# Kernel tuning notes

Hardware: AMD Instinct MI355X
Metric: run time of the kernel (lower is better)

## Reference

```python
import jax, jax.numpy as jnp
import numpy as np

N = 50000
E = 600000
D_IN = 128
D_HID = 128
D_OUT = 40
BN_EPS = 1e-5


def setup_inputs() -> dict:
    key = jax.random.key(0)
    ks = jax.random.split(key, 16)
    g = lambda k, *s: (jax.random.normal(k, s, jnp.float32) * 0.05)
    return {
        "x": jax.random.normal(ks[0], (N, D_IN), jnp.float32),
        "edge_index": jax.random.randint(ks[1], (2, E), 0, N, dtype=jnp.int64),
        "W0": g(ks[2], D_IN, D_HID), "b0": jnp.zeros((D_HID,), jnp.float32),
        "W1": g(ks[3], D_HID, D_HID), "b1": jnp.zeros((D_HID,), jnp.float32),
        "W2": g(ks[4], D_HID, D_OUT), "b2": jnp.zeros((D_OUT,), jnp.float32),
        "g0": 1.0 + g(ks[5], D_HID), "be0": g(ks[6], D_HID),
        "m0": g(ks[7], D_HID), "v0": 0.5 + jax.random.uniform(ks[8], (D_HID,), jnp.float32),
        "g1": 1.0 + g(ks[9], D_HID), "be1": g(ks[10], D_HID),
        "m1": g(ks[11], D_HID), "v1": 0.5 + jax.random.uniform(ks[12], (D_HID,), jnp.float32),
    }


def reference(x, edge_index, W0, b0, W1, b1, W2, b2,
              g0, be0, m0, v0, g1, be1, m1, v1):
    n = x.shape[0]
    loop = jnp.arange(n, dtype=edge_index.dtype)
    # GCN with self-loops: A_hat = A + I, symmetric normalization
    src = jnp.concatenate([edge_index[0], loop])
    dst = jnp.concatenate([edge_index[1], loop])
    deg = jax.ops.segment_sum(jnp.ones_like(dst, jnp.float32), dst, num_segments=n)
    dinv = jax.lax.rsqrt(jnp.maximum(deg, 1.0))
    norm = dinv[src] * dinv[dst]  # [E+N]

    def conv(h, W, b):
        h = h @ W + b                                   # [N, d_out]
        msg = norm[:, None] * h[src]                    # gather + scale
        return jax.ops.segment_sum(msg, dst, num_segments=n)

    def bn_relu(h, g, be, m, v):
        return jax.nn.relu((h - m) * (g * jax.lax.rsqrt(v + BN_EPS)) + be)

    h = bn_relu(conv(x, W0, b0), g0, be0, m0, v0)
    h = bn_relu(conv(h, W1, b1), g1, be1, m1, v1)
    h = conv(h, W2, b2)
    return jax.nn.log_softmax(h, axis=-1)
```

## Files before the change

kernel.cpp:

```cpp
#include <hip/hip_runtime.h>
#include <math.h>

#define BN_EPS 1e-5f
#define CAP 96

typedef unsigned short ushort_t;
typedef __attribute__((ext_vector_type(8))) short short8;
typedef __attribute__((ext_vector_type(4))) float floatx4;

__device__ inline ushort_t f2b(float f) {
    unsigned u = __float_as_uint(f);
    unsigned r = u + 0x7FFFu + ((u >> 16) & 1u);
    return (ushort_t)(r >> 16);
}
__device__ inline float b2f(ushort_t b) { return __uint_as_float(((unsigned)b) << 16); }
__device__ inline float2 u2f2(unsigned u) {
    return make_float2(b2f((ushort_t)(u & 0xffffu)), b2f((ushort_t)(u >> 16)));
}


__global__ void fill_ell(const int* __restrict__ ei, int* __restrict__ cnt,
                         int* __restrict__ ell, int E) {
    int e = blockIdx.x * blockDim.x + threadIdx.x;
    if (e >= E) return;
    int s = ei[e];
    int d = ei[E + e];
    int p = atomicAdd(&cnt[d], 1);
    if (p < CAP) ell[(size_t)d * CAP + p] = s;
}

__global__ void make_dinv(const int* __restrict__ cnt, float* __restrict__ dinv, int n) {
    int i = blockIdx.x * blockDim.x + threadIdx.x;
    if (i < n) dinv[i] = rsqrtf((float)(cnt[i] + 1));
}

__global__ __launch_bounds__(256) void cast_wt_all(const float* __restrict__ W0,
                                                   const float* __restrict__ W1,
                                                   const float* __restrict__ W2,
                                                   ushort_t* __restrict__ Wt0,
                                                   ushort_t* __restrict__ Wt1,
                                                   ushort_t* __restrict__ Wt2) {
    int i = blockIdx.x * 256 + threadIdx.x;
    if (i < 16384) {
        int n = i >> 7, k = i & 127;
        Wt0[i] = f2b(W0[k * 128 + n]);
    } else if (i < 32768) {
        int j = i - 16384;
        int n = j >> 7, k = j & 127;
        Wt1[j] = f2b(W1[k * 128 + n]);
    } else if (i < 40960) {
        int j = i - 32768;
        int n = j >> 7, k = j & 127;
        Wt2[j] = (n < 40) ? f2b(W2[k * 40 + n]) : (ushort_t)0;
    }
}

template<int NT, bool AF32>
__global__ __launch_bounds__(256) void gemm_mfma(const void* __restrict__ Av,
                                                 const ushort_t* __restrict__ Wt,
                                                 const float* __restrict__ bias,
                                                 const float* __restrict__ dinv,
                                                 ushort_t* __restrict__ C,
                                                 int M, int ncols) {
    __shared__ ushort_t As[128 * 128];
    __shared__ ushort_t Ws[NT * 128];
    const int tid = threadIdx.x;
    const int rbase = blockIdx.x * 128;

#pragma unroll
    for (int p = 0; p < 8; ++p) {
        int cid = p * 256 + tid;
        int gr = rbase + (cid >> 4);
        if (AF32) {
            const float* A32 = (const float*)Av;
            float4 f0 = make_float4(0.f, 0.f, 0.f, 0.f), f1 = f0;
            if (gr < M) {
                f0 = *(const float4*)(A32 + (size_t)rbase * 128 + (size_t)cid * 8);
                f1 = *(const float4*)(A32 + (size_t)rbase * 128 + (size_t)cid * 8 + 4);
            }
            union { ushort_t u[8]; uint4 w; } o;
            o.u[0] = f2b(f0.x); o.u[1] = f2b(f0.y); o.u[2] = f2b(f0.z); o.u[3] = f2b(f0.w);
            o.u[4] = f2b(f1.x); o.u[5] = f2b(f1.y); o.u[6] = f2b(f1.z); o.u[7] = f2b(f1.w);
            *(uint4*)(As + cid * 8) = o.w;
        } else {
            const ushort_t* A16 = (const ushort_t*)Av;
            uint4 val = make_uint4(0, 0, 0, 0);
            if (gr < M) val = *(const uint4*)(A16 + (size_t)rbase * 128 + (size_t)cid * 8);
            *(uint4*)(As + cid * 8) = val;
        }
    }
#pragma unroll
    for (int p = 0; p < NT / 16; ++p) {
        int cid = p * 256 + tid;
        *(uint4*)(Ws + cid * 8) = *(const uint4*)(Wt + (size_t)cid * 8);
    }
    __syncthreads();

    const int wave = tid >> 6, lane = tid & 63;
    const int m = lane & 15, quad = lane >> 4;
    constexpr int CT = NT / 16;
    floatx4 acc[2][CT];
#pragma unroll
    for (int rt = 0; rt < 2; ++rt)
#pragma unroll
        for (int ct = 0; ct < CT; ++ct) acc[rt][ct] = (floatx4){0.f, 0.f, 0.f, 0.f};

    const int r0 = wave * 32;
#pragma unroll
    for (int ks = 0; ks < 4; ++ks) {
        short8 a0 = *(const short8*)(As + (r0 + m) * 128 + ks * 32 + quad * 8);
        short8 a1 = *(const short8*)(As + (r0 + 16 + m) * 128 + ks * 32 + quad * 8);
#pragma unroll
        for (int ct = 0; ct < CT; ++ct) {
            short8 b = *(const short8*)(Ws + (ct * 16 + m) * 128 + ks * 32 + quad * 8);
            acc[0][ct] = __builtin_amdgcn_mfma_f32_16x16x32_bf16(a0, b, acc[0][ct], 0, 0, 0);
            acc[1][ct] = __builtin_amdgcn_mfma_f32_16x16x32_bf16(a1, b, acc[1][ct], 0, 0, 0);
        }
    }

    float dsc[2][4];
#pragma unroll
    for (int rt = 0; rt < 2; ++rt)
#pragma unroll
        for (int r = 0; r < 4; ++r) {
            int gr = rbase + r0 + rt * 16 + quad * 4 + r;
            dsc[rt][r] = (gr < M) ? dinv[gr] : 0.f;
        }

    __syncthreads();
#pragma unroll
    for (int rt = 0; rt < 2; ++rt) {
#pragma unroll
        for (int ct = 0; ct < CT; ++ct) {
            int col = ct * 16 + m;
            float bv = (col < ncols) ? bias[col] : 0.f;
#pragma unroll
            for (int r = 0; r < 4; ++r) {
                int row = r0 + rt * 16 + quad * 4 + r;
                As[row * NT + col] = f2b((acc[rt][ct][r] + bv) * dsc[rt][r]);
            }
        }
    }
    __syncthreads();
    constexpr int CPT = 128 * NT / 8 / 256;
#pragma unroll
    for (int p = 0; p < CPT; ++p) {
        int cid = p * 256 + tid;
        int row = cid / (NT / 8);
        int gr = rbase + row;
        if (gr < M)
            *(uint4*)(C + (size_t)gr * NT + (cid % (NT / 8)) * 8) = *(const uint4*)(As + cid * 8);
    }
}

__global__ __launch_bounds__(256) void agg128_bn(const ushort_t* __restrict__ h,
                                                 const int* __restrict__ cnt,
                                                 const int* __restrict__ ell,
                                                 const float* __restrict__ dinv,
                                                 const float* __restrict__ g,
                                                 const float* __restrict__ be,
                                                 const float* __restrict__ m,
                                                 const float* __restrict__ v,
                                                 ushort_t* __restrict__ out, int n) {
    int wv = __builtin_amdgcn_readfirstlane((blockIdx.x * 256 + threadIdx.x) >> 6);
    int lane = threadIdx.x & 63;
    if (wv >= n) return;
    const unsigned* h2 = (const unsigned*)h;
    float dv = dinv[wv];
    float2 hv = u2f2(h2[(size_t)wv * 64 + lane]);
    float ax = hv.x, ay = hv.y;
    int c = min(cnt[wv], CAP);
    const int* row = ell + (size_t)wv * CAP;
    int k = 0;
    for (; k + 8 <= c; k += 8) {
        int s[8];
#pragma unroll
        for (int j = 0; j < 8; ++j) s[j] = row[k + j];
#pragma unroll
        for (int j = 0; j < 8; ++j) {
            float2 t = u2f2(h2[(size_t)s[j] * 64 + lane]);
            ax += t.x;
            ay += t.y;
        }
    }
    if (k < c) {
        int rem = c - k;
        int s[8];
#pragma unroll
        for (int j = 0; j < 8; ++j) {
            int sr = row[k + j];
            s[j] = (j < rem) ? sr : 0;
        }
#pragma unroll
        for (int j = 0; j < 8; ++j) {
            float2 t = u2f2(h2[(size_t)s[j] * 64 + lane]);
            ax += (j < rem) ? t.x : 0.f;
            ay += (j < rem) ? t.y : 0.f;
        }
    }
    ax *= dv;
    ay *= dv;
    int c0 = lane * 2;
    float s0f = g[c0] * rsqrtf(v[c0] + BN_EPS);
    float s1f = g[c0 + 1] * rsqrtf(v[c0 + 1] + BN_EPS);
    float o0 = fmaxf(fmaf(ax - m[c0], s0f, be[c0]), 0.f);
    float o1 = fmaxf(fmaf(ay - m[c0 + 1], s1f, be[c0 + 1]), 0.f);
    unsigned ov = (unsigned)f2b(o0) | ((unsigned)f2b(o1) << 16);
    ((unsigned*)out)[(size_t)wv * 64 + lane] = ov;
}

__global__ __launch_bounds__(256) void agg40_lsm(const ushort_t* __restrict__ h,
                                                 const int* __restrict__ cnt,
                                                 const int* __restrict__ ell,
                                                 const float* __restrict__ dinv,
                                                 float* __restrict__ out, int n) {
    int wv = __builtin_amdgcn_readfirstlane((blockIdx.x * 256 + threadIdx.x) >> 6);
    int lane = threadIdx.x & 63;
    if (wv >= n) return;
    float dv = dinv[wv];
    float acc = b2f(h[(size_t)wv * 64 + lane]);
    int c = min(cnt[wv], CAP);
    const int* row = ell + (size_t)wv * CAP;
    int k = 0;
    for (; k + 8 <= c; k += 8) {
        int s[8];
#pragma unroll
        for (int j = 0; j < 8; ++j) s[j] = row[k + j];
#pragma unroll
        for (int j = 0; j < 8; ++j) acc += b2f(h[(size_t)s[j] * 64 + lane]);
    }
    if (k < c) {
        int rem = c - k;
        int s[8];
#pragma unroll
        for (int j = 0; j < 8; ++j) {
            int sr = row[k + j];
            s[j] = (j < rem) ? sr : 0;
        }
#pragma unroll
        for (int j = 0; j < 8; ++j) {
            float t = b2f(h[(size_t)s[j] * 64 + lane]);
            acc += (j < rem) ? t : 0.f;
        }
    }
    acc *= dv;
    bool act = lane < 40;
    float x = act ? acc : -INFINITY;
    float mx = x;
#pragma unroll
    for (int off = 32; off > 0; off >>= 1) mx = fmaxf(mx, __shfl_xor(mx, off, 64));
    float ex = act ? expf(acc - mx) : 0.f;
    float se = ex;
#pragma unroll
    for (int off = 32; off > 0; off >>= 1) se += __shfl_xor(se, off, 64);
    float r = acc - mx - logf(se);
    if (act) out[(size_t)wv * 40 + lane] = r;
}


extern "C" void kernel_launch(void* const* d_in, const int* in_sizes, int n_in,
                              void* d_out, int out_size, void* d_ws, size_t ws_size,
                              hipStream_t stream) {
    const float* x = (const float*)d_in[0];
    const int* ei = (const int*)d_in[1];
    const float* W0 = (const float*)d_in[2];
    const float* b0 = (const float*)d_in[3];
    const float* W1 = (const float*)d_in[4];
    const float* b1 = (const float*)d_in[5];
    const float* W2 = (const float*)d_in[6];
    const float* b2 = (const float*)d_in[7];
    const float* g0 = (const float*)d_in[8];
    const float* be0 = (const float*)d_in[9];
    const float* m0 = (const float*)d_in[10];
    const float* v0 = (const float*)d_in[11];
    const float* g1 = (const float*)d_in[12];
    const float* be1 = (const float*)d_in[13];
    const float* m1 = (const float*)d_in[14];
    const float* v1 = (const float*)d_in[15];
    float* out = (float*)d_out;

    const int N = in_sizes[0] / 128;
    const int E = in_sizes[1] / 2;

    char* wp = (char*)d_ws;
    auto alloc = [&](size_t bytes) -> char* {
        char* p = wp;
        wp += (bytes + 255) & ~(size_t)255;
        return p;
    };
    int* cnt = (int*)alloc((size_t)N * 4);
    float* dinv = (float*)alloc((size_t)N * 4);
    int* ell = (int*)alloc(((size_t)N * CAP + 8) * 4);
    ushort_t* hA = (ushort_t*)alloc((size_t)N * 128 * 2);
    ushort_t* hB = (ushort_t*)alloc((size_t)N * 128 * 2);
    ushort_t* hA2 = (ushort_t*)alloc((size_t)N * 128 * 2);
    ushort_t* hB2 = (ushort_t*)alloc((size_t)N * 128 * 2);
    ushort_t* hL = (ushort_t*)alloc((size_t)N * 64 * 2);
    ushort_t* Wt0 = (ushort_t*)alloc(128 * 128 * 2);
    ushort_t* Wt1 = (ushort_t*)alloc(128 * 128 * 2);
    ushort_t* Wt2 = (ushort_t*)alloc(64 * 128 * 2);

    hipMemsetAsync(cnt, 0, (size_t)N * 4, stream);
    fill_ell<<<(E + 255) / 256, 256, 0, stream>>>(ei, cnt, ell, E);
    make_dinv<<<(N + 255) / 256, 256, 0, stream>>>(cnt, dinv, N);
    cast_wt_all<<<160, 256, 0, stream>>>(W0, W1, W2, Wt0, Wt1, Wt2);

    int gblocks = (N + 127) / 128;
    gemm_mfma<128, true><<<gblocks, 256, 0, stream>>>(x, Wt0, b0, dinv, hA, N, 128);
    agg128_bn<<<(N + 3) / 4, 256, 0, stream>>>(hA, cnt, ell, dinv, g0, be0, m0, v0, hB, N);
    gemm_mfma<128, false><<<gblocks, 256, 0, stream>>>(hB, Wt1, b1, dinv, hA2, N, 128);
    agg128_bn<<<(N + 3) / 4, 256, 0, stream>>>(hA2, cnt, ell, dinv, g1, be1, m1, v1, hB2, N);
    gemm_mfma<64, false><<<gblocks, 256, 0, stream>>>(hB2, Wt2, b2, dinv, hL, N, 40);
    agg40_lsm<<<(N + 3) / 4, 256, 0, stream>>>(hL, cnt, ell, dinv, out, N);
}
```

Baseline: 241.5 us.

## Fuse ELL build, first GEMM and weight casts into one launch; fold dinv into aggregation

Result: slower. 288.2 us (+19.3%).

```diff
diff --git a/kernel.cpp b/kernel.cpp
--- a/kernel.cpp
+++ b/kernel.cpp
@@ -18,81 +18,31 @@
     return make_float2(b2f((ushort_t)(u & 0xffffu)), b2f((ushort_t)(u >> 16)));
 }
 
-
-__global__ void fill_ell(const int* __restrict__ ei, int* __restrict__ cnt,
-                         int* __restrict__ ell, int E) {
-    int e = blockIdx.x * blockDim.x + threadIdx.x;
-    if (e >= E) return;
-    int s = ei[e];
-    int d = ei[E + e];
-    int p = atomicAdd(&cnt[d], 1);
-    if (p < CAP) ell[(size_t)d * CAP + p] = s;
-}
-
-__global__ void make_dinv(const int* __restrict__ cnt, float* __restrict__ dinv, int n) {
-    int i = blockIdx.x * blockDim.x + threadIdx.x;
-    if (i < n) dinv[i] = rsqrtf((float)(cnt[i] + 1));
-}
-
-__global__ __launch_bounds__(256) void cast_wt_all(const float* __restrict__ W0,
-                                                   const float* __restrict__ W1,
-                                                   const float* __restrict__ W2,
-                                                   ushort_t* __restrict__ Wt0,
-                                                   ushort_t* __restrict__ Wt1,
-                                                   ushort_t* __restrict__ Wt2) {
-    int i = blockIdx.x * 256 + threadIdx.x;
-    if (i < 16384) {
-        int n = i >> 7, k = i & 127;
-        Wt0[i] = f2b(W0[k * 128 + n]);
-    } else if (i < 32768) {
-        int j = i - 16384;
-        int n = j >> 7, k = j & 127;
-        Wt1[j] = f2b(W1[k * 128 + n]);
-    } else if (i < 40960) {
-        int j = i - 32768;
-        int n = j >> 7, k = j & 127;
-        Wt2[j] = (n < 40) ? f2b(W2[k * 40 + n]) : (ushort_t)0;
-    }
-}
-
-template<int NT, bool AF32>
-__global__ __launch_bounds__(256) void gemm_mfma(const void* __restrict__ Av,
-                                                 const ushort_t* __restrict__ Wt,
-                                                 const float* __restrict__ bias,
-                                                 const float* __restrict__ dinv,
-                                                 ushort_t* __restrict__ C,
-                                                 int M, int ncols) {
-    __shared__ ushort_t As[128 * 128];
-    __shared__ ushort_t Ws[NT * 128];
-    const int tid = threadIdx.x;
-    const int rbase = blockIdx.x * 128;
-
-#pragma unroll
-    for (int p = 0; p < 8; ++p) {
-        int cid = p * 256 + tid;
-        int gr = rbase + (cid >> 4);
-        if (AF32) {
-            const float* A32 = (const float*)Av;
-            float4 f0 = make_float4(0.f, 0.f, 0.f, 0.f), f1 = f0;
-            if (gr < M) {
-                f0 = *(const float4*)(A32 + (size_t)rbase * 128 + (size_t)cid * 8);
-                f1 = *(const float4*)(A32 + (size_t)rbase * 128 + (size_t)cid * 8 + 4);
-            }
-            union { ushort_t u[8]; uint4 w; } o;
-            o.u[0] = f2b(f0.x); o.u[1] = f2b(f0.y); o.u[2] = f2b(f0.z); o.u[3] = f2b(f0.w);
-            o.u[4] = f2b(f1.x); o.u[5] = f2b(f1.y); o.u[6] = f2b(f1.z); o.u[7] = f2b(f1.w);
-            *(uint4*)(As + cid * 8) = o.w;
-        } else {
-            const ushort_t* A16 = (const ushort_t*)Av;
-            uint4 val = make_uint4(0, 0, 0, 0);
-            if (gr < M) val = *(const uint4*)(A16 + (size_t)rbase * 128 + (size_t)cid * 8);
-            *(uint4*)(As + cid * 8) = val;
-        }
-    }
+template<int NT, bool AF32, bool SELFW>
+__device__ __forceinline__ void gemm_body(
+    ushort_t* __restrict__ Ws,
+    const void* __restrict__ Av,
+    const void* __restrict__ Wsrc,
+    const float* __restrict__ bias,
+    ushort_t* __restrict__ C,
+    int M, int ncols, int rbase, int tid)
+{
 #pragma unroll
     for (int p = 0; p < NT / 16; ++p) {
         int cid = p * 256 + tid;
-        *(uint4*)(Ws + cid * 8) = *(const uint4*)(Wt + (size_t)cid * 8);
+        int nr = cid >> 4, seg = cid & 15;
+        ushort_t* dst = Ws + nr * 128 + ((seg ^ (nr & 15)) << 3);
+        if (SELFW) {
+            const float* Wf = (const float*)Wsrc;
+            int k0 = seg * 8;
+            union { ushort_t u[8]; uint4 w; } o;
+#pragma unroll
+            for (int j = 0; j < 8; ++j) o.u[j] = f2b(Wf[(size_t)(k0 + j) * NT + nr]);
+            *(uint4*)dst = o.w;
+        } else {
+            const ushort_t* Wt = (const ushort_t*)Wsrc;
+            *(uint4*)dst = *(const uint4*)(Wt + (size_t)cid * 8);
+        }
     }
     __syncthreads();
 
@@ -106,81 +56,145 @@
         for (int ct = 0; ct < CT; ++ct) acc[rt][ct] = (floatx4){0.f, 0.f, 0.f, 0.f};
 
     const int r0 = wave * 32;
+    const int ra = rbase + r0 + m;
+    const int rb = ra + 16;
+    const bool oka = ra < M, okb = rb < M;
+
 #pragma unroll
     for (int ks = 0; ks < 4; ++ks) {
-        short8 a0 = *(const short8*)(As + (r0 + m) * 128 + ks * 32 + quad * 8);
-        short8 a1 = *(const short8*)(As + (r0 + 16 + m) * 128 + ks * 32 + quad * 8);
+        int ko = ks * 32 + quad * 8;
+        short8 a0 = {0, 0, 0, 0, 0, 0, 0, 0}, a1 = a0;
+        if (AF32) {
+            const float* A32 = (const float*)Av;
+            if (oka) {
+                const float* p = A32 + (size_t)ra * 128 + ko;
+                float4 f0 = *(const float4*)p, f1 = *(const float4*)(p + 4);
+                a0[0] = f2b(f0.x); a0[1] = f2b(f0.y); a0[2] = f2b(f0.z); a0[3] = f2b(f0.w);
+                a0[4] = f2b(f1.x); a0[5] = f2b(f1.y); a0[6] = f2b(f1.z); a0[7] = f2b(f1.w);
+            }
+            if (okb) {
+                const float* p = A32 + (size_t)rb * 128 + ko;
+                float4 f0 = *(const float4*)p, f1 = *(const float4*)(p + 4);
+                a1[0] = f2b(f0.x); a1[1] = f2b(f0.y); a1[2] = f2b(f0.z); a1[3] = f2b(f0.w);
+                a1[4] = f2b(f1.x); a1[5] = f2b(f1.y); a1[6] = f2b(f1.z); a1[7] = f2b(f1.w);
+            }
+        } else {
+            const ushort_t* A16 = (const ushort_t*)Av;
+            if (oka) a0 = *(const short8*)(A16 + (size_t)ra * 128 + ko);
+            if (okb) a1 = *(const short8*)(A16 + (size_t)rb * 128 + ko);
+        }
 #pragma unroll
         for (int ct = 0; ct < CT; ++ct) {
-            short8 b = *(const short8*)(Ws + (ct * 16 + m) * 128 + ks * 32 + quad * 8);
+            short8 b = *(const short8*)(Ws + (ct * 16 + m) * 128 + (((ks * 4 + quad) ^ m) << 3));
             acc[0][ct] = __builtin_amdgcn_mfma_f32_16x16x32_bf16(a0, b, acc[0][ct], 0, 0, 0);
             acc[1][ct] = __builtin_amdgcn_mfma_f32_16x16x32_bf16(a1, b, acc[1][ct], 0, 0, 0);
         }
     }
 
-    float dsc[2][4];
+    __syncthreads();
+    constexpr int SEGN = NT / 8, CMASK = SEGN - 1;
 #pragma unroll
     for (int rt = 0; rt < 2; ++rt)
-#pragma unroll
-        for (int r = 0; r < 4; ++r) {
-            int gr = rbase + r0 + rt * 16 + quad * 4 + r;
-            dsc[rt][r] = (gr < M) ? dinv[gr] : 0.f;
-        }
-
-    __syncthreads();
-#pragma unroll
-    for (int rt = 0; rt < 2; ++rt) {
 #pragma unroll
         for (int ct = 0; ct < CT; ++ct) {
             int col = ct * 16 + m;
             float bv = (col < ncols) ? bias[col] : 0.f;
+            int seg = col >> 3, cl = col & 7;
 #pragma unroll
             for (int r = 0; r < 4; ++r) {
                 int row = r0 + rt * 16 + quad * 4 + r;
-                As[row * NT + col] = f2b((acc[rt][ct][r] + bv) * dsc[rt][r]);
+                Ws[row * NT + ((seg ^ (row & CMASK)) << 3) + cl] = f2b(acc[rt][ct][r] + bv);
             }
         }
-    }
     __syncthreads();
-    constexpr int CPT = 128 * NT / 8 / 256;
+    constexpr int CPT = (128 * SEGN) / 256;
 #pragma unroll
     for (int p = 0; p < CPT; ++p) {
         int cid = p * 256 + tid;
-        int row = cid / (NT / 8);
+        int row = cid / SEGN, seg = cid & CMASK;
         int gr = rbase + row;
         if (gr < M)
-            *(uint4*)(C + (size_t)gr * NT + (cid % (NT / 8)) * 8) = *(const uint4*)(As + cid * 8);
-    }
+            *(uint4*)(C + (size_t)gr * NT + seg * 8) =
+                *(const uint4*)(Ws + row * NT + ((seg ^ (row & CMASK)) << 3));
+    }
+}
+
+__global__ __launch_bounds__(256) void mega1(
+    const float* __restrict__ x, const float* __restrict__ W0, const float* __restrict__ b0,
+    const float* __restrict__ W1, const float* __restrict__ W2,
+    const int* __restrict__ ei, int* __restrict__ cnt, int* __restrict__ ell,
+    ushort_t* __restrict__ Wt1, ushort_t* __restrict__ Wt2, ushort_t* __restrict__ hA,
+    int M, int E, int FB, int GB)
+{
+    __shared__ ushort_t Ws[128 * 128];
+    int bid = blockIdx.x;
+    if (bid < FB) {
+        int e = bid * 256 + threadIdx.x;
+        if (e < E) {
+            int s = ei[e], d = ei[E + e];
+            int p = atomicAdd(&cnt[d], 1);
+            if (p < CAP) ell[(size_t)d * CAP + p] = s;
+        }
+        return;
+    }
+    bid -= FB;
+    if (bid < GB) {
+        gemm_body<128, true, true>(Ws, x, W0, b0, hA, M, 128, bid * 128, threadIdx.x);
+        return;
+    }
+    bid -= GB;
+    int i = bid * 256 + threadIdx.x;
+    if (i < 16384) {
+        int n = i >> 7, k = i & 127;
+        Wt1[i] = f2b(W1[k * 128 + n]);
+    } else if (i < 24576) {
+        int j = i - 16384;
+        int n = j >> 7, k = j & 127;
+        Wt2[j] = (n < 40) ? f2b(W2[k * 40 + n]) : (ushort_t)0;
+    }
+}
+
+template<int NT>
+__global__ __launch_bounds__(256) void gemm_bf16(const ushort_t* __restrict__ A,
+                                                 const ushort_t* __restrict__ Wt,
+                                                 const float* __restrict__ bias,
+                                                 ushort_t* __restrict__ C, int M, int ncols)
+{
+    __shared__ ushort_t Ws[NT * 128];
+    gemm_body<NT, false, false>(Ws, A, Wt, bias, C, M, ncols, blockIdx.x * 128, threadIdx.x);
 }
 
 __global__ __launch_bounds__(256) void agg128_bn(const ushort_t* __restrict__ h,
                                                  const int* __restrict__ cnt,
                                                  const int* __restrict__ ell,
-                                                 const float* __restrict__ dinv,
                                                  const float* __restrict__ g,
                                                  const float* __restrict__ be,
-                                                 const float* __restrict__ m,
+                                                 const float* __restrict__ mB,
                                                  const float* __restrict__ v,
                                                  ushort_t* __restrict__ out, int n) {
     int wv = __builtin_amdgcn_readfirstlane((blockIdx.x * 256 + threadIdx.x) >> 6);
     int lane = threadIdx.x & 63;
     if (wv >= n) return;
     const unsigned* h2 = (const unsigned*)h;
-    float dv = dinv[wv];
+    int cd = cnt[wv];
+    float dv = rsqrtf((float)(cd + 1));
     float2 hv = u2f2(h2[(size_t)wv * 64 + lane]);
-    float ax = hv.x, ay = hv.y;
-    int c = min(cnt[wv], CAP);
+    float ax = dv * hv.x, ay = dv * hv.y;
+    int c = min(cd, CAP);
     const int* row = ell + (size_t)wv * CAP;
     int k = 0;
     for (; k + 8 <= c; k += 8) {
         int s[8];
 #pragma unroll
         for (int j = 0; j < 8; ++j) s[j] = row[k + j];
+        float ds[8];
+#pragma unroll
+        for (int j = 0; j < 8; ++j) ds[j] = rsqrtf((float)(cnt[s[j]] + 1));
 #pragma unroll
         for (int j = 0; j < 8; ++j) {
             float2 t = u2f2(h2[(size_t)s[j] * 64 + lane]);
-            ax += t.x;
-            ay += t.y;
+            ax = fmaf(ds[j], t.x, ax);
+            ay = fmaf(ds[j], t.y, ay);
         }
     }
     if (k < c) {
@@ -191,11 +205,14 @@
             int sr = row[k + j];
             s[j] = (j < rem) ? sr : 0;
         }
+        float ds[8];
+#pragma unroll
+        for (int j = 0; j < 8; ++j) ds[j] = (j < rem) ? rsqrtf((float)(cnt[s[j]] + 1)) : 0.f;
 #pragma unroll
         for (int j = 0; j < 8; ++j) {
             float2 t = u2f2(h2[(size_t)s[j] * 64 + lane]);
-            ax += (j < rem) ? t.x : 0.f;
-            ay += (j < rem) ? t.y : 0.f;
+            ax = fmaf(ds[j], t.x, ax);
+            ay = fmaf(ds[j], t.y, ay);
         }
     }
     ax *= dv;
@@ -203,8 +220,8 @@
     int c0 = lane * 2;
     float s0f = g[c0] * rsqrtf(v[c0] + BN_EPS);
     float s1f = g[c0 + 1] * rsqrtf(v[c0 + 1] + BN_EPS);
-    float o0 = fmaxf(fmaf(ax - m[c0], s0f, be[c0]), 0.f);
-    float o1 = fmaxf(fmaf(ay - m[c0 + 1], s1f, be[c0 + 1]), 0.f);
+    float o0 = fmaxf(fmaf(ax - mB[c0], s0f, be[c0]), 0.f);
+    float o1 = fmaxf(fmaf(ay - mB[c0 + 1], s1f, be[c0 + 1]), 0.f);
     unsigned ov = (unsigned)f2b(o0) | ((unsigned)f2b(o1) << 16);
     ((unsigned*)out)[(size_t)wv * 64 + lane] = ov;
 }
@@ -212,22 +229,25 @@
 __global__ __launch_bounds__(256) void agg40_lsm(const ushort_t* __restrict__ h,
                                                  const int* __restrict__ cnt,
                                                  const int* __restrict__ ell,
-                                                 const float* __restrict__ dinv,
                                                  float* __restrict__ out, int n) {
     int wv = __builtin_amdgcn_readfirstlane((blockIdx.x * 256 + threadIdx.x) >> 6);
     int lane = threadIdx.x & 63;
     if (wv >= n) return;
-    float dv = dinv[wv];
-    float acc = b2f(h[(size_t)wv * 64 + lane]);
-    int c = min(cnt[wv], CAP);
+    int cd = cnt[wv];
+    float dv = rsqrtf((float)(cd + 1));
+    float acc = dv * b2f(h[(size_t)wv * 64 + lane]);
+    int c = min(cd, CAP);
     const int* row = ell + (size_t)wv * CAP;
     int k = 0;
     for (; k + 8 <= c; k += 8) {
         int s[8];
 #pragma unroll
         for (int j = 0; j < 8; ++j) s[j] = row[k + j];
-#pragma unroll
-        for (int j = 0; j < 8; ++j) acc += b2f(h[(size_t)s[j] * 64 + lane]);
+        float ds[8];
+#pragma unroll
+        for (int j = 0; j < 8; ++j) ds[j] = rsqrtf((float)(cnt[s[j]] + 1));
+#pragma unroll
+        for (int j = 0; j < 8; ++j) acc = fmaf(ds[j], b2f(h[(size_t)s[j] * 64 + lane]), acc);
     }
     if (k < c) {
         int rem = c - k;
@@ -237,11 +257,11 @@
             int sr = row[k + j];
             s[j] = (j < rem) ? sr : 0;
         }
-#pragma unroll
-        for (int j = 0; j < 8; ++j) {
-            float t = b2f(h[(size_t)s[j] * 64 + lane]);
-            acc += (j < rem) ? t : 0.f;
-        }
+        float ds[8];
+#pragma unroll
+        for (int j = 0; j < 8; ++j) ds[j] = (j < rem) ? rsqrtf((float)(cnt[s[j]] + 1)) : 0.f;
+#pragma unroll
+        for (int j = 0; j < 8; ++j) acc = fmaf(ds[j], b2f(h[(size_t)s[j] * 64 + lane]), acc);
     }
     acc *= dv;
     bool act = lane < 40;
@@ -289,27 +309,25 @@
         return p;
     };
     int* cnt = (int*)alloc((size_t)N * 4);
-    float* dinv = (float*)alloc((size_t)N * 4);
     int* ell = (int*)alloc(((size_t)N * CAP + 8) * 4);
     ushort_t* hA = (ushort_t*)alloc((size_t)N * 128 * 2);
     ushort_t* hB = (ushort_t*)alloc((size_t)N * 128 * 2);
     ushort_t* hA2 = (ushort_t*)alloc((size_t)N * 128 * 2);
     ushort_t* hB2 = (ushort_t*)alloc((size_t)N * 128 * 2);
     ushort_t* hL = (ushort_t*)alloc((size_t)N * 64 * 2);
-    ushort_t* Wt0 = (ushort_t*)alloc(128 * 128 * 2);
     ushort_t* Wt1 = (ushort_t*)alloc(128 * 128 * 2);
     ushort_t* Wt2 = (ushort_t*)alloc(64 * 128 * 2);
 
+    const int GB = (N + 127) / 128;
+    const int FB = (E + 255) / 256;
+    const int CB = 96;
+
     hipMemsetAsync(cnt, 0, (size_t)N * 4, stream);
-    fill_ell<<<(E + 255) / 256, 256, 0, stream>>>(ei, cnt, ell, E);
-    make_dinv<<<(N + 255) / 256, 256, 0, stream>>>(cnt, dinv, N);
-    cast_wt_all<<<160, 256, 0, stream>>>(W0, W1, W2, Wt0, Wt1, Wt2);
-
-    int gblocks = (N + 127) / 128;
-    gemm_mfma<128, true><<<gblocks, 256, 0, stream>>>(x, Wt0, b0, dinv, hA, N, 128);
-    agg128_bn<<<(N + 3) / 4, 256, 0, stream>>>(hA, cnt, ell, dinv, g0, be0, m0, v0, hB, N);
-    gemm_mfma<128, false><<<gblocks, 256, 0, stream>>>(hB, Wt1, b1, dinv, hA2, N, 128);
-    agg128_bn<<<(N + 3) / 4, 256, 0, stream>>>(hA2, cnt, ell, dinv, g1, be1, m1, v1, hB2, N);
-    gemm_mfma<64, false><<<gblocks, 256, 0, stream>>>(hB2, Wt2, b2, dinv, hL, N, 40);
-    agg40_lsm<<<(N + 3) / 4, 256, 0, stream>>>(hL, cnt, ell, dinv, out, N);
-}
+    mega1<<<FB + GB + CB, 256, 0, stream>>>(x, W0, b0, W1, W2, ei, cnt, ell,
+                                            Wt1, Wt2, hA, N, E, FB, GB);
+    agg128_bn<<<(N + 3) / 4, 256, 0, stream>>>(hA, cnt, ell, g0, be0, m0, v0, hB, N);
+    gemm_bf16<128><<<GB, 256, 0, stream>>>(hB, Wt1, b1, hA2, N, 128);
+    agg128_bn<<<(N + 3) / 4, 256, 0, stream>>>(hA2, cnt, ell, g1, be1, m1, v1, hB2, N);
+    gemm_bf16<64><<<GB, 256, 0, stream>>>(hB2, Wt2, b2, hL, N, 40);
+    agg40_lsm<<<(N + 3) / 4, 256, 0, stream>>>(hL, cnt, ell, out, N);
+}
```

## Use 16-bit ELL indices, load GEMM A from global, swizzle LDS, merge setup kernels

Applied to the files above, without the earlier changes.

Result: faster. 231.8 us (-4.0%).

```diff
diff --git a/kernel.cpp b/kernel.cpp
--- a/kernel.cpp
+++ b/kernel.cpp
@@ -18,29 +18,24 @@
     return make_float2(b2f((ushort_t)(u & 0xffffu)), b2f((ushort_t)(u >> 16)));
 }
 
-
-__global__ void fill_ell(const int* __restrict__ ei, int* __restrict__ cnt,
-                         int* __restrict__ ell, int E) {
-    int e = blockIdx.x * blockDim.x + threadIdx.x;
-    if (e >= E) return;
-    int s = ei[e];
-    int d = ei[E + e];
-    int p = atomicAdd(&cnt[d], 1);
-    if (p < CAP) ell[(size_t)d * CAP + p] = s;
-}
-
-__global__ void make_dinv(const int* __restrict__ cnt, float* __restrict__ dinv, int n) {
-    int i = blockIdx.x * blockDim.x + threadIdx.x;
-    if (i < n) dinv[i] = rsqrtf((float)(cnt[i] + 1));
-}
-
-__global__ __launch_bounds__(256) void cast_wt_all(const float* __restrict__ W0,
-                                                   const float* __restrict__ W1,
-                                                   const float* __restrict__ W2,
-                                                   ushort_t* __restrict__ Wt0,
-                                                   ushort_t* __restrict__ Wt1,
-                                                   ushort_t* __restrict__ Wt2) {
-    int i = blockIdx.x * 256 + threadIdx.x;
+__global__ __launch_bounds__(256) void fill_ell_cast(
+    const int* __restrict__ ei, int* __restrict__ cnt, ushort_t* __restrict__ ell,
+    const float* __restrict__ W0, const float* __restrict__ W1, const float* __restrict__ W2,
+    ushort_t* __restrict__ Wt0, ushort_t* __restrict__ Wt1, ushort_t* __restrict__ Wt2,
+    int E, int FB)
+{
+    int bid = blockIdx.x;
+    if (bid < FB) {
+        int e = bid * 256 + threadIdx.x;
+        if (e < E) {
+            int s = ei[e];
+            int d = ei[E + e];
+            int p = atomicAdd(&cnt[d], 1);
+            if (p < CAP) ell[(size_t)d * CAP + p] = (ushort_t)s;
+        }
+        return;
+    }
+    int i = (bid - FB) * 256 + threadIdx.x;
     if (i < 16384) {
         int n = i >> 7, k = i & 127;
         Wt0[i] = f2b(W0[k * 128 + n]);
@@ -55,6 +50,11 @@
     }
 }
 
+__global__ void make_dinv(const int* __restrict__ cnt, float* __restrict__ dinv, int n) {
+    int i = blockIdx.x * blockDim.x + threadIdx.x;
+    if (i < n) dinv[i] = rsqrtf((float)(cnt[i] + 1));
+}
+
 template<int NT, bool AF32>
 __global__ __launch_bounds__(256) void gemm_mfma(const void* __restrict__ Av,
                                                  const ushort_t* __restrict__ Wt,
@@ -62,37 +62,16 @@
                                                  const float* __restrict__ dinv,
                                                  ushort_t* __restrict__ C,
                                                  int M, int ncols) {
-    __shared__ ushort_t As[128 * 128];
     __shared__ ushort_t Ws[NT * 128];
     const int tid = threadIdx.x;
     const int rbase = blockIdx.x * 128;
 
 #pragma unroll
-    for (int p = 0; p < 8; ++p) {
-        int cid = p * 256 + tid;
-        int gr = rbase + (cid >> 4);
-        if (AF32) {
-            const float* A32 = (const float*)Av;
-            float4 f0 = make_float4(0.f, 0.f, 0.f, 0.f), f1 = f0;
-            if (gr < M) {
-                f0 = *(const float4*)(A32 + (size_t)rbase * 128 + (size_t)cid * 8);
-                f1 = *(const float4*)(A32 + (size_t)rbase * 128 + (size_t)cid * 8 + 4);
-            }
-            union { ushort_t u[8]; uint4 w; } o;
-            o.u[0] = f2b(f0.x); o.u[1] = f2b(f0.y); o.u[2] = f2b(f0.z); o.u[3] = f2b(f0.w);
-            o.u[4] = f2b(f1.x); o.u[5] = f2b(f1.y); o.u[6] = f2b(f1.z); o.u[7] = f2b(f1.w);
-            *(uint4*)(As + cid * 8) = o.w;
-        } else {
-            const ushort_t* A16 = (const ushort_t*)Av;
-            uint4 val = make_uint4(0, 0, 0, 0);
-            if (gr < M) val = *(const uint4*)(A16 + (size_t)rbase * 128 + (size_t)cid * 8);
-            *(uint4*)(As + cid * 8) = val;
-        }
-    }
-#pragma unroll
     for (int p = 0; p < NT / 16; ++p) {
         int cid = p * 256 + tid;
-        *(uint4*)(Ws + cid * 8) = *(const uint4*)(Wt + (size_t)cid * 8);
+        int nr = cid >> 4, seg = cid & 15;
+        *(uint4*)(Ws + nr * 128 + ((seg ^ (nr & 15)) << 3)) =
+            *(const uint4*)(Wt + (size_t)cid * 8);
     }
     __syncthreads();
 
@@ -106,13 +85,36 @@
         for (int ct = 0; ct < CT; ++ct) acc[rt][ct] = (floatx4){0.f, 0.f, 0.f, 0.f};
 
     const int r0 = wave * 32;
+    const int ra = rbase + r0 + m;
+    const int rb = ra + 16;
+    const bool oka = ra < M, okb = rb < M;
+
 #pragma unroll
     for (int ks = 0; ks < 4; ++ks) {
-        short8 a0 = *(const short8*)(As + (r0 + m) * 128 + ks * 32 + quad * 8);
-        short8 a1 = *(const short8*)(As + (r0 + 16 + m) * 128 + ks * 32 + quad * 8);
+        int ko = ks * 32 + quad * 8;
+        short8 a0 = {0, 0, 0, 0, 0, 0, 0, 0}, a1 = a0;
+        if (AF32) {
+            const float* A32 = (const float*)Av;
+            if (oka) {
+                const float* p = A32 + (size_t)ra * 128 + ko;
+                float4 f0 = *(const float4*)p, f1 = *(const float4*)(p + 4);
+                a0[0] = f2b(f0.x); a0[1] = f2b(f0.y); a0[2] = f2b(f0.z); a0[3] = f2b(f0.w);
+                a0[4] = f2b(f1.x); a0[5] = f2b(f1.y); a0[6] = f2b(f1.z); a0[7] = f2b(f1.w);
+            }
+            if (okb) {
+                const float* p = A32 + (size_t)rb * 128 + ko;
+                float4 f0 = *(const float4*)p, f1 = *(const float4*)(p + 4);
+                a1[0] = f2b(f0.x); a1[1] = f2b(f0.y); a1[2] = f2b(f0.z); a1[3] = f2b(f0.w);
+                a1[4] = f2b(f1.x); a1[5] = f2b(f1.y); a1[6] = f2b(f1.z); a1[7] = f2b(f1.w);
+            }
+        } else {
+            const ushort_t* A16 = (const ushort_t*)Av;
+            if (oka) a0 = *(const short8*)(A16 + (size_t)ra * 128 + ko);
+            if (okb) a1 = *(const short8*)(A16 + (size_t)rb * 128 + ko);
+        }
 #pragma unroll
         for (int ct = 0; ct < CT; ++ct) {
-            short8 b = *(const short8*)(Ws + (ct * 16 + m) * 128 + ks * 32 + quad * 8);
+            short8 b = *(const short8*)(Ws + (ct * 16 + m) * 128 + (((ks * 4 + quad) ^ m) << 3));
             acc[0][ct] = __builtin_amdgcn_mfma_f32_16x16x32_bf16(a0, b, acc[0][ct], 0, 0, 0);
             acc[1][ct] = __builtin_amdgcn_mfma_f32_16x16x32_bf16(a1, b, acc[1][ct], 0, 0, 0);
         }
@@ -128,38 +130,41 @@
         }
 
     __syncthreads();
-#pragma unroll
-    for (int rt = 0; rt < 2; ++rt) {
+    constexpr int SEGN = NT / 8, CMASK = SEGN - 1;
+#pragma unroll
+    for (int rt = 0; rt < 2; ++rt)
 #pragma unroll
         for (int ct = 0; ct < CT; ++ct) {
             int col = ct * 16 + m;
             float bv = (col < ncols) ? bias[col] : 0.f;
+            int seg = col >> 3, cl = col & 7;
 #pragma unroll
             for (int r = 0; r < 4; ++r) {
                 int row = r0 + rt * 16 + quad * 4 + r;
-                As[row * NT + col] = f2b((acc[rt][ct][r] + bv) * dsc[rt][r]);
+                Ws[row * NT + ((seg ^ (row & CMASK)) << 3) + cl] =
+                    f2b((acc[rt][ct][r] + bv) * dsc[rt][r]);
             }
         }
-    }
     __syncthreads();
-    constexpr int CPT = 128 * NT / 8 / 256;
+    constexpr int CPT = (128 * SEGN) / 256;
 #pragma unroll
     for (int p = 0; p < CPT; ++p) {
         int cid = p * 256 + tid;
-        int row = cid / (NT / 8);
+        int row = cid / SEGN, seg = cid & CMASK;
         int gr = rbase + row;
         if (gr < M)
-            *(uint4*)(C + (size_t)gr * NT + (cid % (NT / 8)) * 8) = *(const uint4*)(As + cid * 8);
+            *(uint4*)(C + (size_t)gr * NT + seg * 8) =
+                *(const uint4*)(Ws + row * NT + ((seg ^ (row & CMASK)) << 3));
     }
 }
 
 __global__ __launch_bounds__(256) void agg128_bn(const ushort_t* __restrict__ h,
                                                  const int* __restrict__ cnt,
-                                                 const int* __restrict__ ell,
+                                                 const ushort_t* __restrict__ ell,
                                                  const float* __restrict__ dinv,
                                                  const float* __restrict__ g,
                                                  const float* __restrict__ be,
-                                                 const float* __restrict__ m,
+                                                 const float* __restrict__ mB,
                                                  const float* __restrict__ v,
                                                  ushort_t* __restrict__ out, int n) {
     int wv = __builtin_amdgcn_readfirstlane((blockIdx.x * 256 + threadIdx.x) >> 6);
@@ -170,7 +175,7 @@
     float2 hv = u2f2(h2[(size_t)wv * 64 + lane]);
     float ax = hv.x, ay = hv.y;
     int c = min(cnt[wv], CAP);
-    const int* row = ell + (size_t)wv * CAP;
+    const ushort_t* row = ell + (size_t)wv * CAP;
     int k = 0;
     for (; k + 8 <= c; k += 8) {
         int s[8];
@@ -203,15 +208,15 @@
     int c0 = lane * 2;
     float s0f = g[c0] * rsqrtf(v[c0] + BN_EPS);
     float s1f = g[c0 + 1] * rsqrtf(v[c0 + 1] + BN_EPS);
-    float o0 = fmaxf(fmaf(ax - m[c0], s0f, be[c0]), 0.f);
-    float o1 = fmaxf(fmaf(ay - m[c0 + 1], s1f, be[c0 + 1]), 0.f);
+    float o0 = fmaxf(fmaf(ax - mB[c0], s0f, be[c0]), 0.f);
+    float o1 = fmaxf(fmaf(ay - mB[c0 + 1], s1f, be[c0 + 1]), 0.f);
     unsigned ov = (unsigned)f2b(o0) | ((unsigned)f2b(o1) << 16);
     ((unsigned*)out)[(size_t)wv * 64 + lane] = ov;
 }
 
 __global__ __launch_bounds__(256) void agg40_lsm(const ushort_t* __restrict__ h,
                                                  const int* __restrict__ cnt,
-                                                 const int* __restrict__ ell,
+                                                 const ushort_t* __restrict__ ell,
                                                  const float* __restrict__ dinv,
                                                  float* __restrict__ out, int n) {
     int wv = __builtin_amdgcn_readfirstlane((blockIdx.x * 256 + threadIdx.x) >> 6);
@@ -220,7 +225,7 @@
     float dv = dinv[wv];
     float acc = b2f(h[(size_t)wv * 64 + lane]);
     int c = min(cnt[wv], CAP);
-    const int* row = ell + (size_t)wv * CAP;
+    const ushort_t* row = ell + (size_t)wv * CAP;
     int k = 0;
     for (; k + 8 <= c; k += 8) {
         int s[8];
@@ -290,7 +295,7 @@
     };
     int* cnt = (int*)alloc((size_t)N * 4);
     float* dinv = (float*)alloc((size_t)N * 4);
-    int* ell = (int*)alloc(((size_t)N * CAP + 8) * 4);
+    ushort_t* ell = (ushort_t*)alloc(((size_t)N * CAP + 16) * 2);
     ushort_t* hA = (ushort_t*)alloc((size_t)N * 128 * 2);
     ushort_t* hB = (ushort_t*)alloc((size_t)N * 128 * 2);
     ushort_t* hA2 = (ushort_t*)alloc((size_t)N * 128 * 2);
@@ -300,16 +305,19 @@
     ushort_t* Wt1 = (ushort_t*)alloc(128 * 128 * 2);
     ushort_t* Wt2 = (ushort_t*)alloc(64 * 128 * 2);
 
+    const int GB = (N + 127) / 128;
+    const int FB = (E + 255) / 256;
+    const int CB = 160;
+
     hipMemsetAsync(cnt, 0, (size_t)N * 4, stream);
-    fill_ell<<<(E + 255) / 256, 256, 0, stream>>>(ei, cnt, ell, E);
+    fill_ell_cast<<<FB + CB, 256, 0, stream>>>(ei, cnt, ell, W0, W1, W2,
+                                               Wt0, Wt1, Wt2, E, FB);
     make_dinv<<<(N + 255) / 256, 256, 0, stream>>>(cnt, dinv, N);
-    cast_wt_all<<<160, 256, 0, stream>>>(W0, W1, W2, Wt0, Wt1, Wt2);
-
-    int gblocks = (N + 127) / 128;
-    gemm_mfma<128, true><<<gblocks, 256, 0, stream>>>(x, Wt0, b0, dinv, hA, N, 128);
+
+    gemm_mfma<128, true><<<GB, 256, 0, stream>>>(x, Wt0, b0, dinv, hA, N, 128);
     agg128_bn<<<(N + 3) / 4, 256, 0, stream>>>(hA, cnt, ell, dinv, g0, be0, m0, v0, hB, N);
-    gemm_mfma<128, false><<<gblocks, 256, 0, stream>>>(hB, Wt1, b1, dinv, hA2, N, 128);
+    gemm_mfma<128, false><<<GB, 256, 0, stream>>>(hB, Wt1, b1, dinv, hA2, N, 128);
     agg128_bn<<<(N + 3) / 4, 256, 0, stream>>>(hA2, cnt, ell, dinv, g1, be1, m1, v1, hB2, N);
-    gemm_mfma<64, false><<<gblocks, 256, 0, stream>>>(hB2, Wt2, b2, dinv, hL, N, 40);
+    gemm_mfma<64, false><<<GB, 256, 0, stream>>>(hB2, Wt2, b2, dinv, hL, N, 40);
     agg40_lsm<<<(N + 3) / 4, 256, 0, stream>>>(hL, cnt, ell, dinv, out, N);
 }
```
